# Kernel tuning notes

Measured on AMD Instinct MI355X. Metric: run time of the kernel, lower is better.

## Reference

```python
import jax, jax.numpy as jnp
import numpy as np

B, VIN, C_IN = 8, 4096, 64
VOUT, E, S, C_OUT = 16384, 49152, 9, 32


def setup_inputs() -> dict:
    key = jax.random.key(0)
    ks = jax.random.split(key, 10)
    x = jax.random.normal(ks[0], (B, VIN, C_IN), dtype=jnp.float32)
    trans_row = jax.random.randint(ks[1], (E,), 0, VOUT)  # unused in math (matches original)
    trans_col = jax.random.randint(ks[2], (E,), 0, VIN)
    trans_value = jax.random.uniform(ks[3], (E,), dtype=jnp.float32)
    row_map = jax.random.randint(ks[4], (VOUT, 3), 0, E)
    indices = jax.random.randint(ks[5], (VOUT, S), 0, VOUT)  # spiral neighbor indices
    Wd = jax.random.normal(ks[6], (C_IN, S), dtype=jnp.float32) * 0.1  # depthwise kernel
    bd = jax.random.normal(ks[7], (C_IN,), dtype=jnp.float32) * 0.1
    Wp = jax.random.normal(ks[8], (C_OUT, C_IN), dtype=jnp.float32) * 0.1  # pointwise linear
    bp = jax.random.normal(ks[9], (C_OUT,), dtype=jnp.float32) * 0.1
    return {"x": x, "trans_row": trans_row, "trans_col": trans_col,
            "trans_value": trans_value, "row_map": row_map, "indices": indices,
            "Wd": Wd, "bd": bd, "Wp": Wp, "bp": bp}


def reference(x, trans_row, trans_col, trans_value, row_map, indices, Wd, bd, Wp, bp):
    # --- Pool: COO gather-scale + 3-way gather-and-sum ---
    edge = x[:, trans_col, :] * trans_value[None, :, None]          # [B, E, C]
    pooled = (edge[:, row_map[:, 0], :]
              + edge[:, row_map[:, 1], :]
              + edge[:, row_map[:, 2], :])                          # [B, Vout, C]
    # --- DSConv: spiral gather -> depthwise reduce over spiral -> pointwise ---
    sp = pooled[:, indices, :]                                      # [B, Vout, S, C]
    dw = jnp.einsum('bvsc,cs->bvc', sp, Wd) + bd                    # depthwise Conv2d(C,C,[1,S],groups=C)
    pw = jnp.einsum('bvc,oc->bvo', dw, Wp) + bp                     # pointwise Linear
    return jax.nn.relu(pw)                                          # [B, Vout, C_out]
```

## Files before the change

kernel.cpp:

```cpp
#include <hip/hip_runtime.h>

#define BATCH   8
#define VIN     4096
#define CIN     64
#define VOUTN   16384
#define SN      9
#define COUT    32
#define VT      64

__global__ __launch_bounds__(256) void pool_kernel(
    const float* __restrict__ x, const int* __restrict__ trans_col,
    const float* __restrict__ trans_value, const int* __restrict__ row_map,
    float* __restrict__ pooled) {
  int t  = threadIdx.x;
  int g  = t >> 4;
  int l  = t & 15;
  int b  = blockIdx.x & 7;
  int u  = (blockIdx.x >> 3) * 16 + g;
  const float4* xb4 = (const float4*)(x + (size_t)b * VIN * CIN);
  float4 acc = make_float4(0.f, 0.f, 0.f, 0.f);
#pragma unroll
  for (int j = 0; j < 3; ++j) {
    int   e   = row_map[u * 3 + j];
    int   col = trans_col[e];
    float tv  = trans_value[e];
    float4 p  = xb4[col * 16 + l];
    acc.x += tv * p.x; acc.y += tv * p.y; acc.z += tv * p.z; acc.w += tv * p.w;
  }
  float4* pp = (float4*)(pooled + (size_t)((b << 14) + u) * CIN);
  pp[l] = acc;
}

__global__ __launch_bounds__(256) void dwpw_kernel(
    const float* __restrict__ pooled, const int* __restrict__ indices,
    const float* __restrict__ Wd, const float* __restrict__ bd,
    const float* __restrict__ Wp, const float* __restrict__ bp,
    float* __restrict__ out) {
  __shared__ float dw[VT][65];
  int t = threadIdx.x;
  int b  = blockIdx.x & 7;
  int v0 = (blockIdx.x >> 3) * VT;

  int g  = t >> 4;
  int l  = t & 15;
  int c4 = l * 4;
  float4 wd4[SN];
#pragma unroll
  for (int s = 0; s < SN; ++s) {
    wd4[s].x = Wd[(c4 + 0) * SN + s];
    wd4[s].y = Wd[(c4 + 1) * SN + s];
    wd4[s].z = Wd[(c4 + 2) * SN + s];
    wd4[s].w = Wd[(c4 + 3) * SN + s];
  }
  float4 bd4 = *(const float4*)(bd + c4);
  const float4* pb4 = (const float4*)(pooled + (size_t)(b << 14) * CIN);

#pragma unroll
  for (int vi = 0; vi < 4; ++vi) {
    int vl = g + vi * 16;
    const int* idx = indices + (v0 + vl) * SN;
    float4 acc = bd4;
#pragma unroll
    for (int s = 0; s < SN; ++s) {
      int u = idx[s];
      float4 p = pb4[u * 16 + l];
      acc.x += wd4[s].x * p.x; acc.y += wd4[s].y * p.y;
      acc.z += wd4[s].z * p.z; acc.w += wd4[s].w * p.w;
    }
    dw[vl][c4 + 0] = acc.x; dw[vl][c4 + 1] = acc.y;
    dw[vl][c4 + 2] = acc.z; dw[vl][c4 + 3] = acc.w;
  }
  __syncthreads();

  int vl = t & 63;
  int w  = t >> 6;
  int ob = __builtin_amdgcn_readfirstlane(w * 8);
  float acc[8];
#pragma unroll
  for (int oo = 0; oo < 8; ++oo) acc[oo] = bp[ob + oo];
#pragma unroll 8
  for (int cc = 0; cc < CIN; ++cc) {
    float d = dw[vl][cc];
#pragma unroll
    for (int oo = 0; oo < 8; ++oo)
      acc[oo] += d * Wp[(ob + oo) * CIN + cc];
  }
  float* op = out + (size_t)((b << 14) + v0 + vl) * COUT + ob;
  float4 r0 = make_float4(fmaxf(acc[0], 0.f), fmaxf(acc[1], 0.f),
                          fmaxf(acc[2], 0.f), fmaxf(acc[3], 0.f));
  float4 r1 = make_float4(fmaxf(acc[4], 0.f), fmaxf(acc[5], 0.f),
                          fmaxf(acc[6], 0.f), fmaxf(acc[7], 0.f));
  *(float4*)op = r0;
  *(float4*)(op + 4) = r1;
}

extern "C" void kernel_launch(void* const* d_in, const int* in_sizes, int n_in,
                              void* d_out, int out_size, void* d_ws, size_t ws_size,
                              hipStream_t stream) {
  const float* x    = (const float*)d_in[0];
  const int*   tc   = (const int*)d_in[2];
  const float* tv   = (const float*)d_in[3];
  const int*   rm   = (const int*)d_in[4];
  const int*   idx  = (const int*)d_in[5];
  const float* Wd   = (const float*)d_in[6];
  const float* bd   = (const float*)d_in[7];
  const float* Wp   = (const float*)d_in[8];
  const float* bp   = (const float*)d_in[9];
  float* out = (float*)d_out;
  float* pooled = (float*)d_ws;

  pool_kernel<<<BATCH * (VOUTN / 16), 256, 0, stream>>>(x, tc, tv, rm, pooled);
  dwpw_kernel<<<BATCH * (VOUTN / VT), 256, 0, stream>>>(pooled, idx, Wd, bd, Wp, bp, out);
}
```

Baseline: 126.0 us.

## Store pooled intermediate as bf16 and stage indices and weights in LDS

The pooled intermediate is now written as bf16 instead of fp32, which halves the bytes written by the pool kernel and read by the gather in the dwpw kernel. The pool kernel stages row_map, trans_col and trans_value lookups in shared memory, and the dwpw kernel stages spiral indices and the transposed depthwise weights in LDS so they are loaded with coalesced reads. This cuts memory traffic on the random gathers. In exchange the intermediate loses precision, which may exceed the accuracy tolerance.

Result: faster. 115.4 us (-8.4%).

```diff
diff --git a/kernel.cpp b/kernel.cpp
--- a/kernel.cpp
+++ b/kernel.cpp
@@ -7,65 +7,85 @@
 #define SN      9
 #define COUT    32
 #define VT      64
+#define UPB     16
+
+__device__ __forceinline__ unsigned short f2bf(float f) {
+  unsigned u = __float_as_uint(f);
+  u += 0x7FFFu + ((u >> 16) & 1u);
+  return (unsigned short)(u >> 16);
+}
+__device__ __forceinline__ float bf2f(unsigned short h) {
+  return __uint_as_float((unsigned)h << 16);
+}
 
 __global__ __launch_bounds__(256) void pool_kernel(
     const float* __restrict__ x, const int* __restrict__ trans_col,
     const float* __restrict__ trans_value, const int* __restrict__ row_map,
-    float* __restrict__ pooled) {
+    unsigned short* __restrict__ pooled) {
+  __shared__ int   scol[UPB * 3];
+  __shared__ float sval[UPB * 3];
   int t  = threadIdx.x;
-  int g  = t >> 4;
-  int l  = t & 15;
   int b  = blockIdx.x & 7;
-  int u  = (blockIdx.x >> 3) * 16 + g;
+  int u0 = (blockIdx.x >> 3) * UPB;
+  if (t < UPB * 3) {
+    int e   = row_map[u0 * 3 + t];
+    scol[t] = trans_col[e];
+    sval[t] = trans_value[e];
+  }
+  __syncthreads();
+  int g = t >> 4, l = t & 15;
   const float4* xb4 = (const float4*)(x + (size_t)b * VIN * CIN);
   float4 acc = make_float4(0.f, 0.f, 0.f, 0.f);
 #pragma unroll
   for (int j = 0; j < 3; ++j) {
-    int   e   = row_map[u * 3 + j];
-    int   col = trans_col[e];
-    float tv  = trans_value[e];
+    int   col = scol[g * 3 + j];
+    float tv  = sval[g * 3 + j];
     float4 p  = xb4[col * 16 + l];
     acc.x += tv * p.x; acc.y += tv * p.y; acc.z += tv * p.z; acc.w += tv * p.w;
   }
-  float4* pp = (float4*)(pooled + (size_t)((b << 14) + u) * CIN);
-  pp[l] = acc;
+  ushort4 h;
+  h.x = f2bf(acc.x); h.y = f2bf(acc.y); h.z = f2bf(acc.z); h.w = f2bf(acc.w);
+  ((ushort4*)(pooled + (size_t)((b << 14) + u0 + g) * CIN))[l] = h;
 }
 
 __global__ __launch_bounds__(256) void dwpw_kernel(
-    const float* __restrict__ pooled, const int* __restrict__ indices,
+    const unsigned short* __restrict__ pooled, const int* __restrict__ indices,
     const float* __restrict__ Wd, const float* __restrict__ bd,
     const float* __restrict__ Wp, const float* __restrict__ bp,
     float* __restrict__ out) {
   __shared__ float dw[VT][65];
-  int t = threadIdx.x;
+  __shared__ int   sidx[VT * SN];
+  __shared__ float swdT[SN * CIN];
+  int t  = threadIdx.x;
   int b  = blockIdx.x & 7;
   int v0 = (blockIdx.x >> 3) * VT;
 
-  int g  = t >> 4;
-  int l  = t & 15;
-  int c4 = l * 4;
+  for (int i = t; i < VT * SN; i += 256) {
+    sidx[i] = indices[v0 * SN + i];
+    int c = i / SN, s = i - c * SN;
+    swdT[s * CIN + c] = Wd[i];
+  }
+  __syncthreads();
+
+  int g = t >> 4, l = t & 15, c4 = l * 4;
   float4 wd4[SN];
 #pragma unroll
-  for (int s = 0; s < SN; ++s) {
-    wd4[s].x = Wd[(c4 + 0) * SN + s];
-    wd4[s].y = Wd[(c4 + 1) * SN + s];
-    wd4[s].z = Wd[(c4 + 2) * SN + s];
-    wd4[s].w = Wd[(c4 + 3) * SN + s];
-  }
+  for (int s = 0; s < SN; ++s) wd4[s] = *(const float4*)&swdT[s * CIN + c4];
   float4 bd4 = *(const float4*)(bd + c4);
-  const float4* pb4 = (const float4*)(pooled + (size_t)(b << 14) * CIN);
+  const ushort4* pb4 = (const ushort4*)(pooled + (size_t)(b << 14) * CIN);
 
 #pragma unroll
   for (int vi = 0; vi < 4; ++vi) {
     int vl = g + vi * 16;
-    const int* idx = indices + (v0 + vl) * SN;
     float4 acc = bd4;
 #pragma unroll
     for (int s = 0; s < SN; ++s) {
-      int u = idx[s];
-      float4 p = pb4[u * 16 + l];
-      acc.x += wd4[s].x * p.x; acc.y += wd4[s].y * p.y;
-      acc.z += wd4[s].z * p.z; acc.w += wd4[s].w * p.w;
+      int u = sidx[vl * SN + s];
+      ushort4 h = pb4[u * 16 + l];
+      acc.x += wd4[s].x * bf2f(h.x);
+      acc.y += wd4[s].y * bf2f(h.y);
+      acc.z += wd4[s].z * bf2f(h.z);
+      acc.w += wd4[s].w * bf2f(h.w);
     }
     dw[vl][c4 + 0] = acc.x; dw[vl][c4 + 1] = acc.y;
     dw[vl][c4 + 2] = acc.z; dw[vl][c4 + 3] = acc.w;
@@ -107,8 +127,8 @@
   const float* Wp   = (const float*)d_in[8];
   const float* bp   = (const float*)d_in[9];
   float* out = (float*)d_out;
-  float* pooled = (float*)d_ws;
+  unsigned short* pooled = (unsigned short*)d_ws;
 
-  pool_kernel<<<BATCH * (VOUTN / 16), 256, 0, stream>>>(x, tc, tv, rm, pooled);
+  pool_kernel<<<BATCH * (VOUTN / UPB), 256, 0, stream>>>(x, tc, tv, rm, pooled);
   dwpw_kernel<<<BATCH * (VOUTN / VT), 256, 0, stream>>>(pooled, idx, Wd, bd, Wp, bp, out);
 }
```
